# Kernel tuning notes

Hardware: AMD Instinct MI355X
Metric: run time of the kernel (lower is better)

The kernel has to match this reference:

```python
import math
import jax, jax.numpy as jnp
import numpy as np

B, T, C = 8, 1024, 768
H = 12
D = C // H  # 64


def setup_inputs() -> dict:
    key = jax.random.key(0)
    k1, k2, k3, k4, k5 = jax.random.split(key, 5)
    s = 0.02
    return {
        "x": jax.random.normal(k1, (B, T, C), dtype=jnp.float32),
        "w_qkv": jax.random.normal(k2, (C, 3 * C), dtype=jnp.float32) * s,
        "b_qkv": jax.random.normal(k3, (3 * C,), dtype=jnp.float32) * s,
        "w_proj": jax.random.normal(k4, (C, C), dtype=jnp.float32) * s,
        "b_proj": jax.random.normal(k5, (C,), dtype=jnp.float32) * s,
    }


def reference(x, w_qkv, b_qkv, w_proj, b_proj):
    b, t, c = x.shape
    qkv = x @ w_qkv + b_qkv                      # [B,T,3C]
    q, k, v = jnp.split(qkv, 3, axis=-1)
    # [B,T,C] -> [B,H,T,D]
    q = q.reshape(b, t, H, D).transpose(0, 2, 1, 3)
    k = k.reshape(b, t, H, D).transpose(0, 2, 1, 3)
    v = v.reshape(b, t, H, D).transpose(0, 2, 1, 3)
    scale = 1.0 / math.sqrt(D)
    att = jnp.einsum("bhqd,bhkd->bhqk", q, k) * scale   # [B,H,T,T]
    causal = jnp.tril(jnp.ones((t, t), dtype=bool))
    att = jnp.where(causal, att, -jnp.inf)
    att = jax.nn.softmax(att, axis=-1)
    y = jnp.einsum("bhqk,bhkd->bhqd", att, v)            # [B,H,T,D]
    y = y.transpose(0, 2, 1, 3).reshape(b, t, c)
    return y @ w_proj + b_proj
```

## Files before the change

### kernel.cpp

```cpp
#include <hip/hip_runtime.h>
#include <math.h>

#define B_ 8
#define T_ 1024
#define C_ 768
#define H_ 12
#define D_ 64

typedef __bf16 bf16x8 __attribute__((ext_vector_type(8)));
typedef float  f32x4  __attribute__((ext_vector_type(4)));
typedef unsigned short us8 __attribute__((ext_vector_type(8)));
typedef unsigned int   u32x4v __attribute__((ext_vector_type(4)));

typedef __attribute__((address_space(3))) void lds_void;
typedef __attribute__((address_space(1))) const void glb_void;

#define KSC 0.18033688011112043f

__device__ __forceinline__ unsigned short f2bf(float f) {
    unsigned int u = __float_as_uint(f);
    u += 0x7fffu + ((u >> 16) & 1u);
    return (unsigned short)(u >> 16);
}

__global__ __launch_bounds__(256)
void prep_all(const float* __restrict__ x, const float* __restrict__ w_qkv,
              const float* __restrict__ b_qkv, const float* __restrict__ w_proj,
              unsigned short* __restrict__ xb, unsigned short* __restrict__ wqT,
              unsigned short* __restrict__ wpT, float* __restrict__ bqs) {
    __shared__ unsigned short Ts[64][65];
    const int id  = blockIdx.x;
    const int tid = threadIdx.x;
    if (id < 6144) {
        int idx = id * 256 + tid;
        float4 v = ((const float4*)x)[idx];
        ushort4 o;
        o.x = f2bf(v.x); o.y = f2bf(v.y); o.z = f2bf(v.z); o.w = f2bf(v.w);
        ((ushort4*)xb)[idx] = o;
        return;
    }
    if (id < 6729) {
        const float* W; unsigned short* Wt; int N, nlim, t2;
        if (id < 6576) { t2 = id - 6144; W = w_qkv;  Wt = wqT; N = 3 * C_; nlim = C_;
            ;
        } else if (id < 6720) { t2 = id - 6576; W = w_proj; Wt = wpT; N = C_; nlim = 0;
        } else {
            int i = (id - 6720) * 256 + tid;
            if (i < 3 * C_) bqs[i] = b_qkv[i] * (i < C_ ? KSC : 1.f);
            return;
        }
        const int ntiles = N / 64;
        const int n0 = (t2 % ntiles) * 64, k0 = (t2 / ntiles) * 64;
        for (int i = tid; i < 4096; i += 256) {
            int n = i & 63, k = i >> 6;
            float sc = (n0 + n < nlim) ? KSC : 1.f;
            Ts[n][k] = f2bf(W[(size_t)(k0 + k) * N + n0 + n] * sc);
        }
        __syncthreads();
        for (int i = tid; i < 4096; i += 256) {
            int k = i & 63, n = i >> 6;
            Wt[(size_t)(n0 + n) * 768 + k0 + k] = Ts[n][k];
        }
    }
}

template<int OUT_BF16>
__global__ __launch_bounds__(256)
void gemm_bf16_bt(const unsigned short* __restrict__ A,
                  const unsigned short* __restrict__ Bt,
                  const float* __restrict__ bias,
                  void* __restrict__ Cout,
                  int M, int N, int K) {
    __shared__ __align__(16) unsigned short As[8192];
    __shared__ __align__(16) unsigned short Bs[8192];

    const int tid  = threadIdx.x;
    const int lane = tid & 63;
    const int c    = lane & 15;
    const int quad = lane >> 4;
    const int wave = tid >> 6;
    const int wm   = (wave >> 1) * 64;
    const int wn   = (wave & 1) * 64;
    const int bm   = blockIdx.x * 128;
    const int bn   = blockIdx.y * 128;

    const unsigned short* aS[4];
    const unsigned short* bS[4];
#pragma unroll
    for (int p = 0; p < 4; p++) {
        int Lp = p * 256 + tid;
        int L  = Lp ^ ((Lp >> 3) & 7);
        aS[p] = A  + (size_t)(bm + (L >> 3)) * K + (L & 7) * 8;
        bS[p] = Bt + (size_t)(bn + (L >> 3)) * K + (L & 7) * 8;
    }
    const int wb = (tid & 0xC0) * 8;

    int aoff[4][2], boff[4][2];
#pragma unroll
    for (int i = 0; i < 4; i++)
#pragma unroll
        for (int ks = 0; ks < 2; ks++) {
            const int kcA = (ks * 4 + quad) ^ (c & 7);
            aoff[i][ks] = ((wm + i * 16 + c) * 8 + kcA) * 8;
            boff[i][ks] = ((wn + i * 16 + c) * 8 + kcA) * 8;
        }

    f32x4 acc[4][4];
#pragma unroll
    for (int i = 0; i < 4; i++)
#pragma unroll
        for (int j = 0; j < 4; j++) acc[i][j] = (f32x4){0.f, 0.f, 0.f, 0.f};

    for (int kt = 0; kt < K; kt += 64) {
        __syncthreads();
#pragma unroll
        for (int p = 0; p < 4; p++) {
            __builtin_amdgcn_global_load_lds((glb_void*)aS[p],
                (lds_void*)(As + p * 2048 + wb), 16, 0, 0);
            __builtin_amdgcn_global_load_lds((glb_void*)bS[p],
                (lds_void*)(Bs + p * 2048 + wb), 16, 0, 0);
            aS[p] += 64; bS[p] += 64;
        }
        __syncthreads();
#pragma unroll
        for (int ks = 0; ks < 2; ks++) {
            bf16x8 af[4], bfr[4];
#pragma unroll
            for (int i = 0; i < 4; i++)
                af[i] = __builtin_bit_cast(bf16x8, *(const us8*)&As[aoff[i][ks]]);
#pragma unroll
            for (int j = 0; j < 4; j++)
                bfr[j] = __builtin_bit_cast(bf16x8, *(const us8*)&Bs[boff[j][ks]]);
#pragma unroll
            for (int i = 0; i < 4; i++)
#pragma unroll
                for (int j = 0; j < 4; j++)
                    acc[i][j] = __builtin_amdgcn_mfma_f32_16x16x32_bf16(af[i], bfr[j], acc[i][j], 0, 0, 0);
        }
    }

    float bs[4];
#pragma unroll
    for (int j = 0; j < 4; j++) bs[j] = bias[bn + wn + j * 16 + c];
#pragma unroll
    for (int i = 0; i < 4; i++) {
        const int gm = bm + wm + i * 16 + quad * 4;
#pragma unroll
        for (int r = 0; r < 4; r++) {
            const size_t ro = (size_t)(gm + r) * N;
#pragma unroll
            for (int j = 0; j < 4; j++) {
                const float v = acc[i][j][r] + bs[j];
                const int gn = bn + wn + j * 16 + c;
                if (OUT_BF16) ((unsigned short*)Cout)[ro + gn] = f2bf(v);
                else          ((float*)Cout)[ro + gn] = v;
            }
        }
    }
}

__device__ __forceinline__ int sigmaK(int k) {
    return 16 * (2 * (k >> 5) + ((k >> 2) & 1)) + 4 * ((k >> 3) & 3) + (k & 3);
}

__global__ __launch_bounds__(256, 3)
void attn_mfma(const unsigned short* __restrict__ qkv, unsigned short* __restrict__ y) {
    __shared__ __align__(16) unsigned short Ks[64 * 72];
    __shared__ __align__(16) unsigned int   Vt[64 * 36];

    const int tid  = threadIdx.x;
    const int wave = tid >> 6;
    const int lane = tid & 63;
    const int c    = lane & 15;
    const int quad = lane >> 4;

    const int id = blockIdx.x;
    const int p  = (id >> 3) & 7;
    const int bh = (id >> 6) * 8 + (id & 7);
    const int b  = bh / H_;
    const int h  = bh - b * H_;

    const int qts[2] = {p, 15 - p};
    const int q0s[2] = {p * 64, (15 - p) * 64};

    const int RS = 3 * C_;
    const unsigned short* kbase = qkv + (size_t)b * T_ * RS + C_ + h * D_;
    const unsigned short* vbase = qkv + (size_t)b * T_ * RS + 2 * C_ + h * D_;

    const u32x4v onesu = {0x3F803F80u, 0x3F803F80u, 0x3F803F80u, 0x3F803F80u};
    const bf16x8 onesf = __builtin_bit_cast(bf16x8, onesu);

    bf16x8 qf[2][2];
#pragma unroll
    for (int t = 0; t < 2; t++) {
        const unsigned short* qrow =
            qkv + ((size_t)(b * T_ + q0s[t] + wave * 16 + c)) * RS + h * D_ + quad * 8;
        qf[t][0] = __builtin_bit_cast(bf16x8, *(const us8*)qrow);
        qf[t][1] = __builtin_bit_cast(bf16x8, *(const us8*)(qrow + 32));
    }

    const int kr0 = tid >> 3, kc0 = tid & 7;
    const int sK0 = sigmaK(kr0) * 72 + kc0 * 8;
    const int sK1 = sigmaK(kr0 + 32) * 72 + kc0 * 8;
    const int dg  = tid >> 4, kp0 = tid & 15;

    us8 kA, kB;
    ushort4 vA0, vB0, vA1, vB1;
    {
        kA = *(const us8*)(kbase + (size_t)kr0 * RS + kc0 * 8);
        kB = *(const us8*)(kbase + (size_t)(kr0 + 32) * RS + kc0 * 8);
        const unsigned short* p0 = vbase + (size_t)(2 * kp0) * RS + dg * 4;
        vA0 = *(const ushort4*)p0;  vB0 = *(const ushort4*)(p0 + RS);
        const unsigned short* p1 = vbase + (size_t)(2 * (kp0 + 16)) * RS + dg * 4;
        vA1 = *(const ushort4*)p1;  vB1 = *(const ushort4*)(p1 + RS);
    }

    f32x4 Oa[2][4];
    f32x4 Ol[2];
#pragma unroll
    for (int t = 0; t < 2; t++) {
        Ol[t] = (f32x4){0.f, 0.f, 0.f, 0.f};
#pragma unroll
        for (int d = 0; d < 4; d++) Oa[t][d] = (f32x4){0.f, 0.f, 0.f, 0.f};
    }

    const int ktEnd = qts[1];
    for (int kt = 0; kt <= ktEnd; kt++) {
        __syncthreads();
        *(us8*)&Ks[sK0] = kA;
        *(us8*)&Ks[sK1] = kB;
        {
            unsigned int* v0 = &Vt[(dg * 4) * 36 + kp0];
            v0[0]   = vA0.x | ((unsigned)vB0.x << 16);
            v0[36]  = vA0.y | ((unsigned)vB0.y << 16);
            v0[72]  = vA0.z | ((unsigned)vB0.z << 16);
            v0[108] = vA0.w | ((unsigned)vB0.w << 16);
            unsigned int* v1 = v0 + 16;
            v1[0]   = vA1.x | ((unsigned)vB1.x << 16);
            v1[36]  = vA1.y | ((unsigned)vB1.y << 16);
            v1[72]  = vA1.z | ((unsigned)vB1.z << 16);
            v1[108] = vA1.w | ((unsigned)vB1.w << 16);
        }
        __syncthreads();

        if (kt < ktEnd) {
            const unsigned short* kp = kbase + (size_t)((kt + 1) * 64) * RS;
            kA = *(const us8*)(kp + (size_t)kr0 * RS + kc0 * 8);
            kB = *(const us8*)(kp + (size_t)(kr0 + 32) * RS + kc0 * 8);
            const unsigned short* vp = vbase + (size_t)((kt + 1) * 64) * RS;
            const unsigned short* p0 = vp + (size_t)(2 * kp0) * RS + dg * 4;
            vA0 = *(const ushort4*)p0;  vB0 = *(const ushort4*)(p0 + RS);
            const unsigned short* p1 = vp + (size_t)(2 * (kp0 + 16)) * RS + dg * 4;
            vA1 = *(const ushort4*)p1;  vB1 = *(const ushort4*)(p1 + RS);
        }

        bf16x8 kf[4][2];
#pragma unroll
        for (int nb = 0; nb < 4; nb++) {
#pragma unroll
            for (int ks = 0; ks < 2; ks++)
                kf[nb][ks] = __builtin_bit_cast(bf16x8,
                    *(const us8*)&Ks[(nb * 16 + c) * 72 + quad * 8 + ks * 32]);
        }

#pragma unroll
        for (int t = 0; t < 2; t++) {
            if (kt > qts[t]) continue;
            const bool diag = (kt == qts[t]);
            const bool doHi = !diag || (wave >= 2);
            const int nbmax = diag ? ((wave >= 2) ? 3 : 1) : 3;

            f32x4 sv[4];
#pragma unroll
            for (int nb = 0; nb < 4; nb++) {
                if (nb <= nbmax) {
                    f32x4 z = (f32x4){0.f, 0.f, 0.f, 0.f};
                    z = __builtin_amdgcn_mfma_f32_16x16x32_bf16(kf[nb][0], qf[t][0], z, 0, 0, 0);
                    sv[nb] = __builtin_amdgcn_mfma_f32_16x16x32_bf16(kf[nb][1], qf[t][1], z, 0, 0, 0);
                }
            }
            if (diag) {
                const int qloc = wave * 16 + c;
#pragma unroll
                for (int nb = 0; nb < 4; nb++) {
                    if (nb <= nbmax) {
                        const int kb = 32 * (nb >> 1) + 4 * (nb & 1) + 8 * quad;
#pragma unroll
                        for (int r = 0; r < 4; r++)
                            if (kb + r > qloc) sv[nb][r] = -INFINITY;
                    }
                }
            }

            unsigned int pd[4][2];
#pragma unroll
            for (int nb = 0; nb < 4; nb++) {
                if (nb <= nbmax) {
                    float p0 = __builtin_amdgcn_exp2f(sv[nb][0]);
                    float p1 = __builtin_amdgcn_exp2f(sv[nb][1]);
                    float p2 = __builtin_amdgcn_exp2f(sv[nb][2]);
                    float p3 = __builtin_amdgcn_exp2f(sv[nb][3]);
                    unsigned u0 = __float_as_uint(p0) + 0x8000u;
                    unsigned u1 = __float_as_uint(p1) + 0x8000u;
                    unsigned u2 = __float_as_uint(p2) + 0x8000u;
                    unsigned u3 = __float_as_uint(p3) + 0x8000u;
                    pd[nb][0] = (u0 >> 16) | (u1 & 0xffff0000u);
                    pd[nb][1] = (u2 >> 16) | (u3 & 0xffff0000u);
                } else {
                    pd[nb][0] = 0u; pd[nb][1] = 0u;
                }
            }

            bf16x8 ap0 = __builtin_bit_cast(bf16x8,
                (u32x4v){pd[0][0], pd[0][1], pd[1][0], pd[1][1]});
            bf16x8 ap1 = __builtin_bit_cast(bf16x8,
                (u32x4v){pd[2][0], pd[2][1], pd[3][0], pd[3][1]});

            Ol[t] = __builtin_amdgcn_mfma_f32_16x16x32_bf16(ap0, onesf, Ol[t], 0, 0, 0);
            if (doHi)
                Ol[t] = __builtin_amdgcn_mfma_f32_16x16x32_bf16(ap1, onesf, Ol[t], 0, 0, 0);

#pragma unroll
            for (int dd = 0; dd < 4; dd++) {
                const unsigned int* vrow = &Vt[(dd * 16 + c) * 36 + quad * 4];
                bf16x8 vb0 = __builtin_bit_cast(bf16x8, *(const u32x4v*)vrow);
                Oa[t][dd] = __builtin_amdgcn_mfma_f32_16x16x32_bf16(ap0, vb0, Oa[t][dd], 0, 0, 0);
                if (doHi) {
                    bf16x8 vb1 = __builtin_bit_cast(bf16x8, *(const u32x4v*)(vrow + 16));
                    Oa[t][dd] = __builtin_amdgcn_mfma_f32_16x16x32_bf16(ap1, vb1, Oa[t][dd], 0, 0, 0);
                }
            }
        }
    }

#pragma unroll
    for (int t = 0; t < 2; t++) {
        unsigned short* yrow =
            y + ((size_t)(b * T_ + q0s[t] + wave * 16)) * C_ + h * D_;
#pragma unroll
        for (int r = 0; r < 4; r++) {
            float inv = 1.f / Ol[t][r];
#pragma unroll
            for (int dd = 0; dd < 4; dd++)
                yrow[(size_t)(quad * 4 + r) * C_ + dd * 16 + c] = f2bf(Oa[t][dd][r] * inv);
        }
    }
}

extern "C" void kernel_launch(void* const* d_in, const int* in_sizes, int n_in,
                              void* d_out, int out_size, void* d_ws, size_t ws_size,
                              hipStream_t stream) {
    const float* x      = (const float*)d_in[0];
    const float* w_qkv  = (const float*)d_in[1];
    const float* b_qkv  = (const float*)d_in[2];
    const float* w_proj = (const float*)d_in[3];
    const float* b_proj = (const float*)d_in[4];
    float* out = (float*)d_out;

    unsigned short* xb   = (unsigned short*)d_ws;
    unsigned short* wqT  = xb   + (size_t)B_ * T_ * C_;
    unsigned short* wpT  = wqT  + (size_t)3 * C_ * C_;
    unsigned short* qkvb = wpT  + (size_t)C_ * C_;
    unsigned short* yb   = qkvb + (size_t)B_ * T_ * 3 * C_;
    float*          bqs  = (float*)(yb + (size_t)B_ * T_ * C_);

    prep_all<<<6729, 256, 0, stream>>>(x, w_qkv, b_qkv, w_proj, xb, wqT, wpT, bqs);

    gemm_bf16_bt<1><<<dim3(B_ * T_ / 128, 3 * C_ / 128), 256, 0, stream>>>(
        xb, wqT, bqs, qkvb, B_ * T_, 3 * C_, C_);

    attn_mfma<<<8 * B_ * H_, 256, 0, stream>>>(qkvb, yb);

    gemm_bf16_bt<0><<<dim3(B_ * T_ / 128, C_ / 128), 256, 0, stream>>>(
        yb, wpT, b_proj, out, B_ * T_, C_, C_);
}
```

Baseline: 189.7 us.

## Fuse fp32-to-bf16 input conversion into QKV GEMM and double-buffer B tiles

The separate pass that converted x to bf16 is removed. The QKV GEMM now reads fp32 x directly into registers and converts it to bf16 before storing it in LDS. The GEMM is also restructured to prefetch the next K-tile: B goes into a double-buffered LDS slot and A is held in registers, so loads overlap with the MFMA work, and launch bounds ask for 3 blocks per CU. This drops one full read and write of the activation tensor, but it increases register pressure, and each block re-reads fp32 A across the 18 column tiles, which doubles the A traffic in the GEMM.

```diff
diff --git a/kernel.cpp b/kernel.cpp
--- a/kernel.cpp
+++ b/kernel.cpp
@@ -24,55 +24,42 @@
 }
 
 __global__ __launch_bounds__(256)
-void prep_all(const float* __restrict__ x, const float* __restrict__ w_qkv,
-              const float* __restrict__ b_qkv, const float* __restrict__ w_proj,
-              unsigned short* __restrict__ xb, unsigned short* __restrict__ wqT,
-              unsigned short* __restrict__ wpT, float* __restrict__ bqs) {
+void prep_w(const float* __restrict__ w_qkv, const float* __restrict__ b_qkv,
+            const float* __restrict__ w_proj,
+            unsigned short* __restrict__ wqT, unsigned short* __restrict__ wpT,
+            float* __restrict__ bqs) {
     __shared__ unsigned short Ts[64][65];
     const int id  = blockIdx.x;
     const int tid = threadIdx.x;
-    if (id < 6144) {
-        int idx = id * 256 + tid;
-        float4 v = ((const float4*)x)[idx];
-        ushort4 o;
-        o.x = f2bf(v.x); o.y = f2bf(v.y); o.z = f2bf(v.z); o.w = f2bf(v.w);
-        ((ushort4*)xb)[idx] = o;
+    if (id == 576) {
+        for (int i = tid; i < 3 * C_; i += 256)
+            bqs[i] = b_qkv[i] * (i < C_ ? KSC : 1.f);
         return;
     }
-    if (id < 6729) {
-        const float* W; unsigned short* Wt; int N, nlim, t2;
-        if (id < 6576) { t2 = id - 6144; W = w_qkv;  Wt = wqT; N = 3 * C_; nlim = C_;
-            ;
-        } else if (id < 6720) { t2 = id - 6576; W = w_proj; Wt = wpT; N = C_; nlim = 0;
-        } else {
-            int i = (id - 6720) * 256 + tid;
-            if (i < 3 * C_) bqs[i] = b_qkv[i] * (i < C_ ? KSC : 1.f);
-            return;
-        }
-        const int ntiles = N / 64;
-        const int n0 = (t2 % ntiles) * 64, k0 = (t2 / ntiles) * 64;
-        for (int i = tid; i < 4096; i += 256) {
-            int n = i & 63, k = i >> 6;
-            float sc = (n0 + n < nlim) ? KSC : 1.f;
-            Ts[n][k] = f2bf(W[(size_t)(k0 + k) * N + n0 + n] * sc);
-        }
-        __syncthreads();
-        for (int i = tid; i < 4096; i += 256) {
-            int k = i & 63, n = i >> 6;
-            Wt[(size_t)(n0 + n) * 768 + k0 + k] = Ts[n][k];
-        }
-    }
-}
-
-template<int OUT_BF16>
-__global__ __launch_bounds__(256)
-void gemm_bf16_bt(const unsigned short* __restrict__ A,
-                  const unsigned short* __restrict__ Bt,
-                  const float* __restrict__ bias,
-                  void* __restrict__ Cout,
-                  int M, int N, int K) {
+    const float* W; unsigned short* Wt; int N, nlim, t2;
+    if (id < 432) { t2 = id;       W = w_qkv;  Wt = wqT; N = 3 * C_; nlim = C_; }
+    else          { t2 = id - 432; W = w_proj; Wt = wpT; N = C_;     nlim = 0;  }
+    const int ntiles = N / 64;
+    const int n0 = (t2 % ntiles) * 64, k0 = (t2 / ntiles) * 64;
+    for (int i = tid; i < 4096; i += 256) {
+        int n = i & 63, k = i >> 6;
+        float sc = (n0 + n < nlim) ? KSC : 1.f;
+        Ts[n][k] = f2bf(W[(size_t)(k0 + k) * N + n0 + n] * sc);
+    }
+    __syncthreads();
+    for (int i = tid; i < 4096; i += 256) {
+        int k = i & 63, n = i >> 6;
+        Wt[(size_t)(n0 + n) * 768 + k0 + k] = Ts[n][k];
+    }
+}
+
+template<int A_FP32, int OUT_BF16>
+__global__ __launch_bounds__(256, 3)
+void gemm_pipe(const float* __restrict__ Af, const unsigned short* __restrict__ A16,
+               const unsigned short* __restrict__ Bt, const float* __restrict__ bias,
+               void* __restrict__ Cout, int M, int N, int K) {
     __shared__ __align__(16) unsigned short As[8192];
-    __shared__ __align__(16) unsigned short Bs[8192];
+    __shared__ __align__(16) unsigned short Bs[2][8192];
 
     const int tid  = threadIdx.x;
     const int lane = tid & 63;
@@ -84,13 +71,23 @@
     const int bm   = blockIdx.x * 128;
     const int bn   = blockIdx.y * 128;
 
-    const unsigned short* aS[4];
+    const float*          aF[4];
+    const unsigned short* aH[4];
+    int wAddr[4];
+#pragma unroll
+    for (int p = 0; p < 4; p++) {
+        const int Lp = p * 256 + tid;
+        const int r  = Lp >> 3;
+        const int kc = (Lp ^ r) & 7;
+        if (A_FP32) aF[p] = Af  + (size_t)(bm + r) * K + kc * 8;
+        else        aH[p] = A16 + (size_t)(bm + r) * K + kc * 8;
+        wAddr[p] = Lp * 8;
+    }
     const unsigned short* bS[4];
 #pragma unroll
     for (int p = 0; p < 4; p++) {
-        int Lp = p * 256 + tid;
-        int L  = Lp ^ ((Lp >> 3) & 7);
-        aS[p] = A  + (size_t)(bm + (L >> 3)) * K + (L & 7) * 8;
+        const int Lp = p * 256 + tid;
+        const int L  = Lp ^ ((Lp >> 3) & 7);
         bS[p] = Bt + (size_t)(bn + (L >> 3)) * K + (L & 7) * 8;
     }
     const int wb = (tid & 0xC0) * 8;
@@ -105,23 +102,51 @@
             boff[i][ks] = ((wn + i * 16 + c) * 8 + kcA) * 8;
         }
 
+    float4 a0[4], a1[4];
+    us8    aR[4];
     f32x4 acc[4][4];
 #pragma unroll
     for (int i = 0; i < 4; i++)
 #pragma unroll
         for (int j = 0; j < 4; j++) acc[i][j] = (f32x4){0.f, 0.f, 0.f, 0.f};
 
-    for (int kt = 0; kt < K; kt += 64) {
+#pragma unroll
+    for (int p = 0; p < 4; p++) {
+        __builtin_amdgcn_global_load_lds((glb_void*)bS[p],
+            (lds_void*)(&Bs[0][0] + p * 2048 + wb), 16, 0, 0);
+        bS[p] += 64;
+        if (A_FP32) { a0[p] = *(const float4*)aF[p]; a1[p] = *(const float4*)(aF[p] + 4); aF[p] += 64; }
+        else        { aR[p] = *(const us8*)aH[p]; aH[p] += 64; }
+    }
+
+    const int R = K >> 6;
+    for (int r = 0; r < R; r++) {
         __syncthreads();
 #pragma unroll
         for (int p = 0; p < 4; p++) {
-            __builtin_amdgcn_global_load_lds((glb_void*)aS[p],
-                (lds_void*)(As + p * 2048 + wb), 16, 0, 0);
-            __builtin_amdgcn_global_load_lds((glb_void*)bS[p],
-                (lds_void*)(Bs + p * 2048 + wb), 16, 0, 0);
-            aS[p] += 64; bS[p] += 64;
+            us8 w;
+            if (A_FP32) {
+                w[0] = f2bf(a0[p].x); w[1] = f2bf(a0[p].y);
+                w[2] = f2bf(a0[p].z); w[3] = f2bf(a0[p].w);
+                w[4] = f2bf(a1[p].x); w[5] = f2bf(a1[p].y);
+                w[6] = f2bf(a1[p].z); w[7] = f2bf(a1[p].w);
+            } else w = aR[p];
+            *(us8*)&As[wAddr[p]] = w;
         }
         __syncthreads();
+
+        if (r + 1 < R) {
+#pragma unroll
+            for (int p = 0; p < 4; p++) {
+                __builtin_amdgcn_global_load_lds((glb_void*)bS[p],
+                    (lds_void*)(&Bs[(r + 1) & 1][0] + p * 2048 + wb), 16, 0, 0);
+                bS[p] += 64;
+                if (A_FP32) { a0[p] = *(const float4*)aF[p]; a1[p] = *(const float4*)(aF[p] + 4); aF[p] += 64; }
+                else        { aR[p] = *(const us8*)aH[p]; aH[p] += 64; }
+            }
+        }
+
+        const unsigned short* bbuf = &Bs[r & 1][0];
 #pragma unroll
         for (int ks = 0; ks < 2; ks++) {
             bf16x8 af[4], bfr[4];
@@ -130,7 +155,7 @@
                 af[i] = __builtin_bit_cast(bf16x8, *(const us8*)&As[aoff[i][ks]]);
 #pragma unroll
             for (int j = 0; j < 4; j++)
-                bfr[j] = __builtin_bit_cast(bf16x8, *(const us8*)&Bs[boff[j][ks]]);
+                bfr[j] = __builtin_bit_cast(bf16x8, *(const us8*)&bbuf[boff[j][ks]]);
 #pragma unroll
             for (int i = 0; i < 4; i++)
 #pragma unroll
@@ -357,20 +382,19 @@
     const float* b_proj = (const float*)d_in[4];
     float* out = (float*)d_out;
 
-    unsigned short* xb   = (unsigned short*)d_ws;
-    unsigned short* wqT  = xb   + (size_t)B_ * T_ * C_;
+    unsigned short* wqT  = (unsigned short*)d_ws;
     unsigned short* wpT  = wqT  + (size_t)3 * C_ * C_;
     unsigned short* qkvb = wpT  + (size_t)C_ * C_;
     unsigned short* yb   = qkvb + (size_t)B_ * T_ * 3 * C_;
     float*          bqs  = (float*)(yb + (size_t)B_ * T_ * C_);
 
-    prep_all<<<6729, 256, 0, stream>>>(x, w_qkv, b_qkv, w_proj, xb, wqT, wpT, bqs);
-
-    gemm_bf16_bt<1><<<dim3(B_ * T_ / 128, 3 * C_ / 128), 256, 0, stream>>>(
-        xb, wqT, bqs, qkvb, B_ * T_, 3 * C_, C_);
+    prep_w<<<577, 256, 0, stream>>>(w_qkv, b_qkv, w_proj, wqT, wpT, bqs);
+
+    gemm_pipe<1, 1><<<dim3(B_ * T_ / 128, 3 * C_ / 128), 256, 0, stream>>>(
+        x, nullptr, wqT, bqs, qkvb, B_ * T_, 3 * C_, C_);
 
     attn_mfma<<<8 * B_ * H_, 256, 0, stream>>>(qkvb, yb);
 
-    gemm_bf16_bt<0><<<dim3(B_ * T_ / 128, C_ / 128), 256, 0, stream>>>(
-        yb, wpT, b_proj, out, B_ * T_, C_, C_);
-}
+    gemm_pipe<0, 0><<<dim3(B_ * T_ / 128, C_ / 128), 256, 0, stream>>>(
+        nullptr, yb, wpT, b_proj, out, B_ * T_, C_, C_);
+}
```

New measurement: 183.3 us. -3.4%, faster.

## Double-buffer GEMM tiles and shrink output-projection M tile

Applied to the files above, without the earlier changes.

Replaces the single-buffered GEMM with a double-buffered version. The next K-tile of B is prefetched into the alternate LDS buffer through global_load_lds, and the next A tile is loaded into registers and written to LDS after the MFMA loop, so loads overlap compute. The output projection uses a 64-row M tile, which doubles its grid size for better CU occupancy, and launch bounds request 2 blocks per CU. This costs double LDS use and extra registers for A staging, and the A-path register stores may add latency.

```diff
diff --git a/kernel.cpp b/kernel.cpp
--- a/kernel.cpp
+++ b/kernel.cpp
@@ -39,111 +39,143 @@
         ((ushort4*)xb)[idx] = o;
         return;
     }
-    if (id < 6729) {
-        const float* W; unsigned short* Wt; int N, nlim, t2;
-        if (id < 6576) { t2 = id - 6144; W = w_qkv;  Wt = wqT; N = 3 * C_; nlim = C_;
-            ;
-        } else if (id < 6720) { t2 = id - 6576; W = w_proj; Wt = wpT; N = C_; nlim = 0;
-        } else {
-            int i = (id - 6720) * 256 + tid;
-            if (i < 3 * C_) bqs[i] = b_qkv[i] * (i < C_ ? KSC : 1.f);
-            return;
-        }
-        const int ntiles = N / 64;
-        const int n0 = (t2 % ntiles) * 64, k0 = (t2 / ntiles) * 64;
-        for (int i = tid; i < 4096; i += 256) {
-            int n = i & 63, k = i >> 6;
-            float sc = (n0 + n < nlim) ? KSC : 1.f;
-            Ts[n][k] = f2bf(W[(size_t)(k0 + k) * N + n0 + n] * sc);
-        }
-        __syncthreads();
-        for (int i = tid; i < 4096; i += 256) {
-            int k = i & 63, n = i >> 6;
-            Wt[(size_t)(n0 + n) * 768 + k0 + k] = Ts[n][k];
-        }
-    }
-}
-
-template<int OUT_BF16>
-__global__ __launch_bounds__(256)
-void gemm_bf16_bt(const unsigned short* __restrict__ A,
-                  const unsigned short* __restrict__ Bt,
-                  const float* __restrict__ bias,
-                  void* __restrict__ Cout,
-                  int M, int N, int K) {
-    __shared__ __align__(16) unsigned short As[8192];
-    __shared__ __align__(16) unsigned short Bs[8192];
+    if (id >= 6720) {
+        int i = (id - 6720) * 256 + tid;
+        if (i < 3 * C_) bqs[i] = b_qkv[i] * (i < C_ ? KSC : 1.f);
+        return;
+    }
+    const float* W; unsigned short* Wt; int N, nlim, t2;
+    if (id < 6576) { t2 = id - 6144; W = w_qkv;  Wt = wqT; N = 3 * C_; nlim = C_; }
+    else           { t2 = id - 6576; W = w_proj; Wt = wpT; N = C_;     nlim = 0;  }
+    const int ntiles = N / 64;
+    const int n0 = (t2 % ntiles) * 64, k0 = (t2 / ntiles) * 64;
+    for (int i = tid; i < 4096; i += 256) {
+        int n = i & 63, k = i >> 6;
+        float sc = (n0 + n < nlim) ? KSC : 1.f;
+        Ts[n][k] = f2bf(W[(size_t)(k0 + k) * N + n0 + n] * sc);
+    }
+    __syncthreads();
+    for (int i = tid; i < 4096; i += 256) {
+        int k = i & 63, n = i >> 6;
+        Wt[(size_t)(n0 + n) * 768 + k0 + k] = Ts[n][k];
+    }
+}
+
+template<int TM, int OUT_BF16>
+__global__ __launch_bounds__(256, 2)
+void gemm_db(const unsigned short* __restrict__ A,
+             const unsigned short* __restrict__ Bt,
+             const float* __restrict__ bias,
+             void* __restrict__ Cout, int M, int N, int K) {
+    const int PA = TM / 32;
+    const int MI = TM / 32;
+    __shared__ __align__(16) unsigned short As[2][TM * 64];
+    __shared__ __align__(16) unsigned short Bs[2][8192];
 
     const int tid  = threadIdx.x;
     const int lane = tid & 63;
     const int c    = lane & 15;
     const int quad = lane >> 4;
     const int wave = tid >> 6;
-    const int wm   = (wave >> 1) * 64;
+    const int wm   = (wave >> 1) * (TM / 2);
     const int wn   = (wave & 1) * 64;
-    const int bm   = blockIdx.x * 128;
+    const int bm   = blockIdx.x * TM;
     const int bn   = blockIdx.y * 128;
 
-    const unsigned short* aS[4];
+    const unsigned short* aS[PA];
+    int wA[PA];
+#pragma unroll
+    for (int p = 0; p < PA; p++) {
+        const int Lp = p * 256 + tid;
+        const int L  = Lp ^ ((Lp >> 3) & 7);
+        aS[p] = A + (size_t)(bm + (L >> 3)) * K + (L & 7) * 8;
+        wA[p] = Lp * 8;
+    }
     const unsigned short* bS[4];
 #pragma unroll
     for (int p = 0; p < 4; p++) {
-        int Lp = p * 256 + tid;
-        int L  = Lp ^ ((Lp >> 3) & 7);
-        aS[p] = A  + (size_t)(bm + (L >> 3)) * K + (L & 7) * 8;
+        const int Lp = p * 256 + tid;
+        const int L  = Lp ^ ((Lp >> 3) & 7);
         bS[p] = Bt + (size_t)(bn + (L >> 3)) * K + (L & 7) * 8;
     }
     const int wb = (tid & 0xC0) * 8;
 
-    int aoff[4][2], boff[4][2];
-#pragma unroll
-    for (int i = 0; i < 4; i++)
+    int aoff[MI][2], boff[4][2];
+#pragma unroll
+    for (int i = 0; i < MI; i++)
 #pragma unroll
         for (int ks = 0; ks < 2; ks++) {
             const int kcA = (ks * 4 + quad) ^ (c & 7);
             aoff[i][ks] = ((wm + i * 16 + c) * 8 + kcA) * 8;
-            boff[i][ks] = ((wn + i * 16 + c) * 8 + kcA) * 8;
-        }
-
-    f32x4 acc[4][4];
-#pragma unroll
-    for (int i = 0; i < 4; i++)
+        }
+#pragma unroll
+    for (int j = 0; j < 4; j++)
+#pragma unroll
+        for (int ks = 0; ks < 2; ks++) {
+            const int kcA = (ks * 4 + quad) ^ (c & 7);
+            boff[j][ks] = ((wn + j * 16 + c) * 8 + kcA) * 8;
+        }
+
+    us8 aR[PA];
+    f32x4 acc[MI][4];
+#pragma unroll
+    for (int i = 0; i < MI; i++)
 #pragma unroll
         for (int j = 0; j < 4; j++) acc[i][j] = (f32x4){0.f, 0.f, 0.f, 0.f};
 
-    for (int kt = 0; kt < K; kt += 64) {
+#pragma unroll
+    for (int p = 0; p < PA; p++) { aR[p] = *(const us8*)aS[p]; aS[p] += 64; }
+#pragma unroll
+    for (int p = 0; p < 4; p++) {
+        __builtin_amdgcn_global_load_lds((glb_void*)bS[p],
+            (lds_void*)(&Bs[0][0] + p * 2048 + wb), 16, 0, 0);
+        bS[p] += 64;
+    }
+#pragma unroll
+    for (int p = 0; p < PA; p++) *(us8*)&As[0][wA[p]] = aR[p];
+
+    const int R = K >> 6;
+    for (int r = 0; r < R; r++) {
         __syncthreads();
-#pragma unroll
-        for (int p = 0; p < 4; p++) {
-            __builtin_amdgcn_global_load_lds((glb_void*)aS[p],
-                (lds_void*)(As + p * 2048 + wb), 16, 0, 0);
-            __builtin_amdgcn_global_load_lds((glb_void*)bS[p],
-                (lds_void*)(Bs + p * 2048 + wb), 16, 0, 0);
-            aS[p] += 64; bS[p] += 64;
-        }
-        __syncthreads();
+        const int bb = r & 1, nb = bb ^ 1;
+        if (r + 1 < R) {
+#pragma unroll
+            for (int p = 0; p < PA; p++) { aR[p] = *(const us8*)aS[p]; aS[p] += 64; }
+#pragma unroll
+            for (int p = 0; p < 4; p++) {
+                __builtin_amdgcn_global_load_lds((glb_void*)bS[p],
+                    (lds_void*)(&Bs[nb][0] + p * 2048 + wb), 16, 0, 0);
+                bS[p] += 64;
+            }
+        }
+
 #pragma unroll
         for (int ks = 0; ks < 2; ks++) {
-            bf16x8 af[4], bfr[4];
-#pragma unroll
-            for (int i = 0; i < 4; i++)
-                af[i] = __builtin_bit_cast(bf16x8, *(const us8*)&As[aoff[i][ks]]);
+            bf16x8 af[MI], bfr[4];
+#pragma unroll
+            for (int i = 0; i < MI; i++)
+                af[i] = __builtin_bit_cast(bf16x8, *(const us8*)&As[bb][aoff[i][ks]]);
 #pragma unroll
             for (int j = 0; j < 4; j++)
-                bfr[j] = __builtin_bit_cast(bf16x8, *(const us8*)&Bs[boff[j][ks]]);
-#pragma unroll
-            for (int i = 0; i < 4; i++)
+                bfr[j] = __builtin_bit_cast(bf16x8, *(const us8*)&Bs[bb][boff[j][ks]]);
+#pragma unroll
+            for (int i = 0; i < MI; i++)
 #pragma unroll
                 for (int j = 0; j < 4; j++)
                     acc[i][j] = __builtin_amdgcn_mfma_f32_16x16x32_bf16(af[i], bfr[j], acc[i][j], 0, 0, 0);
         }
+
+        if (r + 1 < R) {
+#pragma unroll
+            for (int p = 0; p < PA; p++) *(us8*)&As[nb][wA[p]] = aR[p];
+        }
     }
 
     float bs[4];
 #pragma unroll
     for (int j = 0; j < 4; j++) bs[j] = bias[bn + wn + j * 16 + c];
 #pragma unroll
-    for (int i = 0; i < 4; i++) {
+    for (int i = 0; i < MI; i++) {
         const int gm = bm + wm + i * 16 + quad * 4;
 #pragma unroll
         for (int r = 0; r < 4; r++) {
@@ -366,11 +398,11 @@
 
     prep_all<<<6729, 256, 0, stream>>>(x, w_qkv, b_qkv, w_proj, xb, wqT, wpT, bqs);
 
-    gemm_bf16_bt<1><<<dim3(B_ * T_ / 128, 3 * C_ / 128), 256, 0, stream>>>(
+    gemm_db<128, 1><<<dim3(B_ * T_ / 128, 3 * C_ / 128), 256, 0, stream>>>(
         xb, wqT, bqs, qkvb, B_ * T_, 3 * C_, C_);
 
     attn_mfma<<<8 * B_ * H_, 256, 0, stream>>>(qkvb, yb);
 
-    gemm_bf16_bt<0><<<dim3(B_ * T_ / 128, C_ / 128), 256, 0, stream>>>(
+    gemm_db<64, 0><<<dim3(B_ * T_ / 64, C_ / 128), 256, 0, stream>>>(
         yb, wpT, b_proj, out, B_ * T_, C_, C_);
 }
```

Result: faster. 185.9 us (-2.0%).
